# Optimization experiments

Hardware: AMD Instinct MI355X
Metric: run time of the kernel (lower is better)

Reference implementation:

```python
import jax, jax.numpy as jnp
import numpy as np

E, I, O = 64, 512, 512
T = 131072
CAP = 3072  # per-expert capacity; E[tokens/expert]=2048, overflow prob ~0 for uniform routing


def setup_inputs() -> dict:
    key = jax.random.key(0)
    k1, k2, k3, k4 = jax.random.split(key, 4)
    x = jax.random.normal(k1, (T, I), dtype=jnp.float32)
    weight = jax.random.normal(k2, (E, O, I), dtype=jnp.float32) * 0.02
    bias = jax.random.normal(k3, (E, O), dtype=jnp.float32) * 0.02
    expert_ids = jax.random.randint(k4, (T,), 0, E, dtype=jnp.int32)
    return {"x": x, "weight": weight, "bias": bias, "expert_ids": expert_ids}


def reference(x, weight, bias, expert_ids):
    # Grouped per-expert linear: y[t] = weight[e[t]] @ x[t] + bias[e[t]]
    # Implemented via capacity-bucketed dispatch -> batched GEMM -> combine.
    num_e, out_f, in_f = weight.shape
    n_tok = x.shape[0]

    order = jnp.argsort(expert_ids)            # tokens sorted by expert
    ids_s = expert_ids[order]
    counts = jax.ops.segment_sum(jnp.ones((n_tok,), jnp.int32), expert_ids,
                                 num_segments=num_e)
    starts = jnp.cumsum(counts) - counts       # exclusive cumsum: group starts
    pos = jnp.arange(n_tok, dtype=jnp.int32) - starts[ids_s]  # rank within expert
    valid = pos < CAP
    # invalid tokens routed to an extra trash row (num_e*CAP)
    slot = jnp.where(valid, ids_s * CAP + pos, num_e * CAP)

    buf = jnp.zeros((num_e * CAP + 1, in_f), x.dtype).at[slot].set(x[order])
    buf = buf[: num_e * CAP].reshape(num_e, CAP, in_f)

    y = jnp.einsum('eci,eoi->eco', buf, weight) + bias[:, None, :]
    y = y.reshape(num_e * CAP, out_f)
    y = jnp.concatenate([y, jnp.zeros((1, out_f), y.dtype)], axis=0)

    y_sorted = y[slot]                          # gather back per sorted token
    out = jnp.zeros((n_tok, out_f), y.dtype).at[order].set(y_sorted)
    return out
```

## Files before the change

kernel.cpp:

```cpp
#include <hip/hip_runtime.h>

constexpr int E = 64, I = 512, O = 512, T = 131072, CAP = 3072;

constexpr int BM = 128, BN = 128, BK = 32;
constexpr int MT = CAP / BM;
constexpr int NT = O / BN;
constexpr int NK = I / BK;
constexpr int LDA = BK + 8;

typedef __bf16 bf16x8 __attribute__((ext_vector_type(8)));
typedef float floatx4 __attribute__((ext_vector_type(4)));

__device__ inline unsigned pack_bf16(float a, float b) {
  unsigned ua = __float_as_uint(a) + 0x8000u;
  unsigned ub = __float_as_uint(b) + 0x8000u;
  return __builtin_amdgcn_perm(ub, ua, 0x07060302);
}

__global__ void scatter_k(const int* __restrict__ ids, int* __restrict__ counts,
                          int* __restrict__ bucket, float* __restrict__ out) {
  int t = blockIdx.x * blockDim.x + threadIdx.x;
  if (t >= T) return;
  int e = ids[t];
  int pos = atomicAdd(&counts[e * 16], 1);
  if (pos < CAP) {
    bucket[e * CAP + pos] = t;
  } else {
    float4 z = make_float4(0.f, 0.f, 0.f, 0.f);
    float* op = out + (size_t)t * O;
    for (int i = 0; i < O; i += 4) *(float4*)(op + i) = z;
  }
}

__global__ __launch_bounds__(256) void moe_gemm(
    const float* __restrict__ x, const float* __restrict__ w,
    const float* __restrict__ bias, const int* __restrict__ counts,
    const int* __restrict__ bucket, float* __restrict__ out) {
  const int bid = blockIdx.x;
  const int e  = bid / (MT * NT);
  const int mt = (bid / NT) % MT;
  const int nt = bid % NT;

  int cnt = counts[e * 16];
  if (cnt > CAP) cnt = CAP;
  if (mt * BM >= cnt) return;

  __shared__ __align__(16) short As[BM * LDA];
  __shared__ __align__(16) short Bs[BN * LDA];
  __shared__ int toks[BM];

  const int t = threadIdx.x;
  if (t < BM) {
    int g = mt * BM + t;
    toks[t] = (g < cnt) ? bucket[e * CAP + g] : -1;
  }
  __syncthreads();

  const int c4 = t & 7;
  const int rb = t >> 3;

  const float* aptr[4];
  const float* bptr[4];
#pragma unroll
  for (int j = 0; j < 4; ++j) {
    int r = rb + 32 * j;
    int tk = toks[r]; if (tk < 0) tk = 0;
    aptr[j] = x + (size_t)tk * I + (c4 << 2);
    bptr[j] = w + (size_t)e * (O * I) + (size_t)(nt * BN + r) * I + (c4 << 2);
  }

  const int lane = t & 63;
  const int wv = t >> 6;
  const int wm = wv >> 1, wn = wv & 1;
  const int lrow = lane & 15;
  const int quad = lane >> 4;

  floatx4 acc[4][4] = {};

  int aoff[4], boff[4];
#pragma unroll
  for (int mmi = 0; mmi < 4; ++mmi)
    aoff[mmi] = (wm * 64 + mmi * 16 + lrow) * LDA + quad * 8;
#pragma unroll
  for (int nni = 0; nni < 4; ++nni)
    boff[nni] = (wn * 64 + nni * 16 + lrow) * LDA + quad * 8;
  const int wroff0 = rb * LDA + (c4 << 2);

  float4 av[2][4], bv[2][4];
#pragma unroll
  for (int j = 0; j < 4; ++j) {
    av[0][j] = *(const float4*)aptr[j];
    bv[0][j] = *(const float4*)bptr[j];
  }

#pragma unroll
  for (int kk = 0; kk < NK; ++kk) {
    const int cur = kk & 1, nxt = cur ^ 1;
    __syncthreads();
#pragma unroll
    for (int j = 0; j < 4; ++j) {
      float4 f = av[cur][j];
      *(uint2*)&As[wroff0 + j * 32 * LDA] =
          make_uint2(pack_bf16(f.x, f.y), pack_bf16(f.z, f.w));
    }
#pragma unroll
    for (int j = 0; j < 4; ++j) {
      float4 f = bv[cur][j];
      *(uint2*)&Bs[wroff0 + j * 32 * LDA] =
          make_uint2(pack_bf16(f.x, f.y), pack_bf16(f.z, f.w));
    }
    if (kk + 1 < NK) {
#pragma unroll
      for (int j = 0; j < 4; ++j) {
        aptr[j] += BK; bptr[j] += BK;
        av[nxt][j] = *(const float4*)aptr[j];
        bv[nxt][j] = *(const float4*)bptr[j];
      }
    }
    __syncthreads();

    bf16x8 af[4], bfr[4];
#pragma unroll
    for (int mmi = 0; mmi < 4; ++mmi) af[mmi] = *(const bf16x8*)&As[aoff[mmi]];
#pragma unroll
    for (int nni = 0; nni < 4; ++nni) bfr[nni] = *(const bf16x8*)&Bs[boff[nni]];
#pragma unroll
    for (int mmi = 0; mmi < 4; ++mmi)
#pragma unroll
      for (int nni = 0; nni < 4; ++nni)
        acc[mmi][nni] = __builtin_amdgcn_mfma_f32_16x16x32_bf16(
            af[mmi], bfr[nni], acc[mmi][nni], 0, 0, 0);
  }

  float bb[4];
#pragma unroll
  for (int nni = 0; nni < 4; ++nni)
    bb[nni] = bias[e * O + nt * BN + wn * 64 + nni * 16 + lrow];

  const int colbase = nt * BN + wn * 64 + lrow;
#pragma unroll
  for (int mmi = 0; mmi < 4; ++mmi) {
    const int rl = wm * 64 + mmi * 16 + quad * 4;
#pragma unroll
    for (int i = 0; i < 4; ++i) {
      const int tk = toks[rl + i];
      if (tk >= 0) {
        float* op = out + (size_t)tk * O + colbase;
#pragma unroll
        for (int nni = 0; nni < 4; ++nni)
          op[nni * 16] = acc[mmi][nni][i] + bb[nni];
      }
    }
  }
}

extern "C" void kernel_launch(void* const* d_in, const int* in_sizes, int n_in,
                              void* d_out, int out_size, void* d_ws, size_t ws_size,
                              hipStream_t stream) {
  const float* x    = (const float*)d_in[0];
  const float* w    = (const float*)d_in[1];
  const float* bias = (const float*)d_in[2];
  const int*   ids  = (const int*)d_in[3];
  float* out = (float*)d_out;

  int* counts = (int*)d_ws;
  int* bucket = counts + 16 * E;

  hipMemsetAsync(counts, 0, 16 * E * sizeof(int), stream);
  scatter_k<<<dim3(T / 256), dim3(256), 0, stream>>>(ids, counts, bucket, out);
  moe_gemm<<<dim3(E * MT * NT), dim3(256), 0, stream>>>(x, w, bias, counts, bucket, out);
}
```

Measured before the change: 655.2 us.

## Use direct global-to-LDS loads, pre-convert weights to bf16, swizzle LDS, remap blocks to XCDs

Replaces the register-staged fp32 loads and bf16 packing with global_load_lds DMA into double-buffered, XOR-swizzled LDS tiles, converting A to bf16 only when reading LDS fragments. When the workspace is large enough, a separate kernel first converts the weights to bf16 so B tiles are half the size. Block indices are remapped so the four N-tiles of each M-tile land on the same XCD to share x rows in L2, and launch bounds request 3 blocks per CU. The cost is an extra full-weight conversion pass on every call and larger fp32 A tiles in LDS.

```diff
diff --git a/kernel.cpp b/kernel.cpp
--- a/kernel.cpp
+++ b/kernel.cpp
@@ -6,7 +6,6 @@
 constexpr int MT = CAP / BM;
 constexpr int NT = O / BN;
 constexpr int NK = I / BK;
-constexpr int LDA = BK + 8;
 
 typedef __bf16 bf16x8 __attribute__((ext_vector_type(8)));
 typedef float floatx4 __attribute__((ext_vector_type(4)));
@@ -16,6 +15,11 @@
   unsigned ub = __float_as_uint(b) + 0x8000u;
   return __builtin_amdgcn_perm(ub, ua, 0x07060302);
 }
+
+#define GLL16(g, s)                                                        \
+  __builtin_amdgcn_global_load_lds(                                        \
+      (const __attribute__((address_space(1))) unsigned int*)(g),          \
+      (__attribute__((address_space(3))) unsigned int*)(s), 16, 0, 0)
 
 __global__ void scatter_k(const int* __restrict__ ids, int* __restrict__ counts,
                           int* __restrict__ bucket, float* __restrict__ out) {
@@ -32,104 +36,154 @@
   }
 }
 
-__global__ __launch_bounds__(256) void moe_gemm(
+__global__ void convw_k(const float4* __restrict__ w, uint2* __restrict__ wb) {
+  int i = blockIdx.x * blockDim.x + threadIdx.x;
+  float4 f = w[i];
+  wb[i] = make_uint2(pack_bf16(f.x, f.y), pack_bf16(f.z, f.w));
+}
+
+template <bool WBF>
+__global__ __launch_bounds__(256, 3) void moe_gemm(
     const float* __restrict__ x, const float* __restrict__ w,
-    const float* __restrict__ bias, const int* __restrict__ counts,
-    const int* __restrict__ bucket, float* __restrict__ out) {
+    const __bf16* __restrict__ wb, const float* __restrict__ bias,
+    const int* __restrict__ counts, const int* __restrict__ bucket,
+    float* __restrict__ out) {
   const int bid = blockIdx.x;
-  const int e  = bid / (MT * NT);
-  const int mt = (bid / NT) % MT;
-  const int nt = bid % NT;
+  const int xcd = bid & 7;
+  const int q8 = bid >> 3;
+  const int nt = q8 & 3;
+  const int G = (q8 >> 2) * 8 + xcd;
+  const int e = G / MT;
+  const int mt = G - e * MT;
 
   int cnt = counts[e * 16];
+  if (cnt < 0) cnt = 0;
   if (cnt > CAP) cnt = CAP;
   if (mt * BM >= cnt) return;
 
-  __shared__ __align__(16) short As[BM * LDA];
-  __shared__ __align__(16) short Bs[BN * LDA];
+  __shared__ __align__(16) float As[2][BM * BK];
+  __shared__ __align__(16) char BsRaw[2][BM * BK * (WBF ? 2 : 4)];
   __shared__ int toks[BM];
 
   const int t = threadIdx.x;
+  const int lane = t & 63;
+  const int wv = t >> 6;
+
   if (t < BM) {
     int g = mt * BM + t;
     toks[t] = (g < cnt) ? bucket[e * CAP + g] : -1;
   }
   __syncthreads();
 
-  const int c4 = t & 7;
-  const int rb = t >> 3;
-
-  const float* aptr[4];
-  const float* bptr[4];
+  const float* asrc[4];
 #pragma unroll
   for (int j = 0; j < 4; ++j) {
-    int r = rb + 32 * j;
-    int tk = toks[r]; if (tk < 0) tk = 0;
-    aptr[j] = x + (size_t)tk * I + (c4 << 2);
-    bptr[j] = w + (size_t)e * (O * I) + (size_t)(nt * BN + r) * I + (c4 << 2);
-  }
-
-  const int lane = t & 63;
-  const int wv = t >> 6;
+    int row = j * 32 + wv * 8 + (lane >> 3);
+    int tk = toks[row];
+    if (tk < 0) tk = 0;
+    int sq = (lane & 7) ^ (row & 7);
+    asrc[j] = x + (size_t)tk * I + sq * 4;
+  }
+
+  const __bf16* bsrcb[2];
+  const float* bsrcf[4];
+  if constexpr (WBF) {
+#pragma unroll
+    for (int j = 0; j < 2; ++j) {
+      int row = j * 64 + wv * 16 + (lane >> 2);
+      int sq = (lane & 3) ^ (row & 3);
+      bsrcb[j] = wb + (size_t)(e * O + nt * BN + row) * I + sq * 8;
+    }
+  } else {
+#pragma unroll
+    for (int j = 0; j < 4; ++j) {
+      int row = j * 32 + wv * 8 + (lane >> 3);
+      int sq = (lane & 7) ^ (row & 7);
+      bsrcf[j] = w + (size_t)(e * O + nt * BN + row) * I + sq * 4;
+    }
+  }
+
+  auto stage = [&](int buf, int kk) {
+#pragma unroll
+    for (int j = 0; j < 4; ++j)
+      GLL16(asrc[j] + kk * BK, &As[buf][(j * 32 + wv * 8) * BK]);
+    if constexpr (WBF) {
+      __bf16* Bs = (__bf16*)BsRaw[buf];
+#pragma unroll
+      for (int j = 0; j < 2; ++j)
+        GLL16(bsrcb[j] + kk * BK, &Bs[(j * 64 + wv * 16) * BK]);
+    } else {
+      float* Bs = (float*)BsRaw[buf];
+#pragma unroll
+      for (int j = 0; j < 4; ++j)
+        GLL16(bsrcf[j] + kk * BK, &Bs[(j * 32 + wv * 8) * BK]);
+    }
+  };
+
   const int wm = wv >> 1, wn = wv & 1;
   const int lrow = lane & 15;
-  const int quad = lane >> 4;
+  const int qd = lane >> 4;
 
   floatx4 acc[4][4] = {};
 
-  int aoff[4], boff[4];
-#pragma unroll
-  for (int mmi = 0; mmi < 4; ++mmi)
-    aoff[mmi] = (wm * 64 + mmi * 16 + lrow) * LDA + quad * 8;
-#pragma unroll
-  for (int nni = 0; nni < 4; ++nni)
-    boff[nni] = (wn * 64 + nni * 16 + lrow) * LDA + quad * 8;
-  const int wroff0 = rb * LDA + (c4 << 2);
-
-  float4 av[2][4], bv[2][4];
-#pragma unroll
-  for (int j = 0; j < 4; ++j) {
-    av[0][j] = *(const float4*)aptr[j];
-    bv[0][j] = *(const float4*)bptr[j];
-  }
+  stage(0, 0);
+  __syncthreads();
 
 #pragma unroll
   for (int kk = 0; kk < NK; ++kk) {
-    const int cur = kk & 1, nxt = cur ^ 1;
-    __syncthreads();
-#pragma unroll
-    for (int j = 0; j < 4; ++j) {
-      float4 f = av[cur][j];
-      *(uint2*)&As[wroff0 + j * 32 * LDA] =
-          make_uint2(pack_bf16(f.x, f.y), pack_bf16(f.z, f.w));
-    }
-#pragma unroll
-    for (int j = 0; j < 4; ++j) {
-      float4 f = bv[cur][j];
-      *(uint2*)&Bs[wroff0 + j * 32 * LDA] =
-          make_uint2(pack_bf16(f.x, f.y), pack_bf16(f.z, f.w));
-    }
-    if (kk + 1 < NK) {
-#pragma unroll
-      for (int j = 0; j < 4; ++j) {
-        aptr[j] += BK; bptr[j] += BK;
-        av[nxt][j] = *(const float4*)aptr[j];
-        bv[nxt][j] = *(const float4*)bptr[j];
+    const int cur = kk & 1;
+    if (kk + 1 < NK) stage(cur ^ 1, kk + 1);
+
+    bf16x8 af[4], bfr[4];
+#pragma unroll
+    for (int mmi = 0; mmi < 4; ++mmi) {
+      const int row = wm * 64 + mmi * 16 + lrow;
+      const int s = row & 7;
+      const float4 c0 =
+          *(const float4*)&As[cur][row * BK + (((2 * qd) ^ s) << 2)];
+      const float4 c1 =
+          *(const float4*)&As[cur][row * BK + (((2 * qd + 1) ^ s) << 2)];
+      bf16x8 a;
+      a[0] = (__bf16)c0.x; a[1] = (__bf16)c0.y;
+      a[2] = (__bf16)c0.z; a[3] = (__bf16)c0.w;
+      a[4] = (__bf16)c1.x; a[5] = (__bf16)c1.y;
+      a[6] = (__bf16)c1.z; a[7] = (__bf16)c1.w;
+      af[mmi] = a;
+    }
+    if constexpr (WBF) {
+      const __bf16* Bs = (const __bf16*)BsRaw[cur];
+#pragma unroll
+      for (int nni = 0; nni < 4; ++nni) {
+        const int row = wn * 64 + nni * 16 + lrow;
+        bfr[nni] = *(const bf16x8*)&Bs[row * BK + ((qd ^ (row & 3)) << 3)];
       }
-    }
-    __syncthreads();
-
-    bf16x8 af[4], bfr[4];
-#pragma unroll
-    for (int mmi = 0; mmi < 4; ++mmi) af[mmi] = *(const bf16x8*)&As[aoff[mmi]];
-#pragma unroll
-    for (int nni = 0; nni < 4; ++nni) bfr[nni] = *(const bf16x8*)&Bs[boff[nni]];
+    } else {
+      const float* Bs = (const float*)BsRaw[cur];
+#pragma unroll
+      for (int nni = 0; nni < 4; ++nni) {
+        const int row = wn * 64 + nni * 16 + lrow;
+        const int s = row & 7;
+        const float4 c0 =
+            *(const float4*)&Bs[row * BK + (((2 * qd) ^ s) << 2)];
+        const float4 c1 =
+            *(const float4*)&Bs[row * BK + (((2 * qd + 1) ^ s) << 2)];
+        bf16x8 b;
+        b[0] = (__bf16)c0.x; b[1] = (__bf16)c0.y;
+        b[2] = (__bf16)c0.z; b[3] = (__bf16)c0.w;
+        b[4] = (__bf16)c1.x; b[5] = (__bf16)c1.y;
+        b[6] = (__bf16)c1.z; b[7] = (__bf16)c1.w;
+        bfr[nni] = b;
+      }
+    }
+
 #pragma unroll
     for (int mmi = 0; mmi < 4; ++mmi)
 #pragma unroll
       for (int nni = 0; nni < 4; ++nni)
         acc[mmi][nni] = __builtin_amdgcn_mfma_f32_16x16x32_bf16(
             af[mmi], bfr[nni], acc[mmi][nni], 0, 0, 0);
+
+    __syncthreads();
   }
 
   float bb[4];
@@ -140,7 +194,7 @@
   const int colbase = nt * BN + wn * 64 + lrow;
 #pragma unroll
   for (int mmi = 0; mmi < 4; ++mmi) {
-    const int rl = wm * 64 + mmi * 16 + quad * 4;
+    const int rl = wm * 64 + mmi * 16 + qd * 4;
 #pragma unroll
     for (int i = 0; i < 4; ++i) {
       const int tk = toks[rl + i];
@@ -155,18 +209,30 @@
 }
 
 extern "C" void kernel_launch(void* const* d_in, const int* in_sizes, int n_in,
-                              void* d_out, int out_size, void* d_ws, size_t ws_size,
-                              hipStream_t stream) {
-  const float* x    = (const float*)d_in[0];
-  const float* w    = (const float*)d_in[1];
+                              void* d_out, int out_size, void* d_ws,
+                              size_t ws_size, hipStream_t stream) {
+  const float* x = (const float*)d_in[0];
+  const float* w = (const float*)d_in[1];
   const float* bias = (const float*)d_in[2];
-  const int*   ids  = (const int*)d_in[3];
+  const int* ids = (const int*)d_in[3];
   float* out = (float*)d_out;
 
   int* counts = (int*)d_ws;
   int* bucket = counts + 16 * E;
+  __bf16* wbuf = (__bf16*)(bucket + E * CAP);
+  const size_t need =
+      (size_t)(16 * E + E * CAP) * sizeof(int) + (size_t)E * O * I * 2;
 
   hipMemsetAsync(counts, 0, 16 * E * sizeof(int), stream);
   scatter_k<<<dim3(T / 256), dim3(256), 0, stream>>>(ids, counts, bucket, out);
-  moe_gemm<<<dim3(E * MT * NT), dim3(256), 0, stream>>>(x, w, bias, counts, bucket, out);
-}
+
+  if (ws_size >= need) {
+    convw_k<<<dim3(E * O * I / 4 / 256), dim3(256), 0, stream>>>(
+        (const float4*)w, (uint2*)wbuf);
+    moe_gemm<true><<<dim3(E * MT * NT), dim3(256), 0, stream>>>(
+        x, w, wbuf, bias, counts, bucket, out);
+  } else {
+    moe_gemm<false><<<dim3(E * MT * NT), dim3(256), 0, stream>>>(
+        x, w, nullptr, bias, counts, bucket, out);
+  }
+}
```

Result: no change. 644.0 us (-1.7%).
